# Kernel tuning notes

Hardware: AMD Instinct MI355X
Metric: run time of the kernel (lower is better)

## Reference

```python
import jax, jax.numpy as jnp
import numpy as np

N = 100000   # nodes
D = 128      # feature dim (in == hidden)
R = 3        # num edge types (relations)
E = 500000   # edges per relation
B = 2        # num bases


def setup_inputs() -> dict:
    key = jax.random.key(0)
    ks = jax.random.split(key, 12)
    s = 1.0 / np.sqrt(D)  # xavier-ish scale
    return {
        "x": jax.random.normal(ks[0], (N, D), jnp.float32),
        "edge_src": jax.random.randint(ks[1], (R, E), 0, N, dtype=jnp.int32),
        "edge_dst": jax.random.randint(ks[2], (R, E), 0, N, dtype=jnp.int32),
        "proj_w": jax.random.normal(ks[3], (D, D), jnp.float32) * s,
        "proj_b": jnp.zeros((D,), jnp.float32),
        "basis1": jax.random.normal(ks[4], (B, D, D), jnp.float32) * s,
        "coeff1": jax.random.normal(ks[5], (R, B), jnp.float32),
        "bias1": jnp.zeros((D,), jnp.float32),
        "loop1": jax.random.normal(ks[6], (D, D), jnp.float32) * s,
        "basis2": jax.random.normal(ks[7], (B, D, D), jnp.float32) * s,
        "coeff2": jax.random.normal(ks[8], (R, B), jnp.float32),
        "bias2": jnp.zeros((D,), jnp.float32),
        "loop2": jax.random.normal(ks[9], (D, D), jnp.float32) * s,
    }


def rel_graph_conv_layer(x, edge_src, edge_dst, basis, coeff, bias, loop_w):
    """RelGraphConvLayer: per-relation GraphConv(norm='right') + basis weights
    + self-loop + bias + relu. x: [N, D]."""
    # Offset dst ids per relation so one segment_sum covers all R relations.
    seg = (edge_dst + jnp.arange(R, dtype=edge_dst.dtype)[:, None] * N).reshape(-1)  # [R*E]
    gathered = x[edge_src.reshape(-1)]  # [R*E, D]
    agg = jax.ops.segment_sum(gathered, seg, num_segments=R * N).reshape(R, N, D)
    deg = jax.ops.segment_sum(jnp.ones((R * E,), x.dtype), seg, num_segments=R * N).reshape(R, N, 1)
    agg = agg / jnp.maximum(deg, 1.0)  # norm='right': 1/in_degree, clamped to >=1
    W = jnp.einsum('rb,bio->rio', coeff, basis)          # basis decomposition [R, D, D]
    h = jnp.einsum('rnd,rdo->no', agg, W)                # sum over relations (HeteroGraphConv 'sum')
    h = h + x @ loop_w + bias                            # self-loop + bias
    return jax.nn.relu(h)


def reference(x, edge_src, edge_dst, proj_w, proj_b,
              basis1, coeff1, bias1, loop1,
              basis2, coeff2, bias2, loop2):
    h = x @ proj_w + proj_b  # per-ntype projection layer
    h = rel_graph_conv_layer(h, edge_src, edge_dst, basis1, coeff1, bias1, loop1)
    h = rel_graph_conv_layer(h, edge_src, edge_dst, basis2, coeff2, bias2, loop2)
    return h
```

## Files before the change

### kernel.cpp

```cpp
#include <hip/hip_runtime.h>

typedef unsigned int uint;
typedef unsigned short ushort;
typedef __attribute__((ext_vector_type(8))) short bf16x8;
typedef __attribute__((ext_vector_type(4))) float f32x4;

namespace {
constexpr int kN = 100000;
constexpr int kD = 128;
constexpr int kR = 3;
constexpr int kE = 500000;
constexpr int kB = 2;
constexpr int kRN = kR * kN;
constexpr int kRE = kR * kE;
constexpr int kKS = kR * kD;
constexpr int kKC = kD + kKS;
constexpr int kNBK = (kN + 511) / 512;
constexpr int kNQ = kR * kNBK;
constexpr int kCB = (kRE + 2047) / 2048;
constexpr int kBCAP = 4096;
constexpr int kICAP = 5120;
}

__device__ __forceinline__ ushort f2bf(float f) {
    uint u = __builtin_bit_cast(uint, f);
    u += 0x7fff + ((u >> 16) & 1);
    return (ushort)(u >> 16);
}
__device__ __forceinline__ float bf2f(ushort h) {
    return __builtin_bit_cast(float, (uint)h << 16);
}
__device__ __forceinline__ int rel_of(int i) {
    return (i >= kE) + (i >= 2 * kE);
}

__device__ __forceinline__ void gload16(const void* g, void* l) {
    __builtin_amdgcn_global_load_lds(
        (__attribute__((address_space(1))) void*)(g),
        (__attribute__((address_space(3))) void*)(l),
        16, 0, 0);
}

__global__ __launch_bounds__(256)
void init_kernel(unsigned* __restrict__ bcur)
{
    const int q = blockIdx.x * 256 + threadIdx.x;
    if (q < kNQ) bcur[q] = (unsigned)q * kBCAP;
}

__global__ __launch_bounds__(256)
void f2bf_kernel(const float* __restrict__ in, ushort* __restrict__ out)
{
    const int i = blockIdx.x * 256 + threadIdx.x;
    const float4 v = ((const float4*)in)[i];
    ushort4 o;
    o.x = f2bf(v.x); o.y = f2bf(v.y); o.z = f2bf(v.z); o.w = f2bf(v.w);
    ((ushort4*)out)[i] = o;
}

__global__ __launch_bounds__(256)
void passB_kernel(const int* __restrict__ src, const int* __restrict__ dst,
                  unsigned* __restrict__ bcur, uint* __restrict__ colbkt)
{
    __shared__ unsigned bl[kNQ];
    __shared__ unsigned base_l[kNQ];
    const int tid = threadIdx.x;
    for (int q = tid; q < kNQ; q += 256) bl[q] = 0;
    __syncthreads();
    const int i0 = blockIdx.x * 2048 + tid * 8;
    int dd[8], qq[8];
    const bool full = (i0 + 8 <= kRE);
    if (full) {
        const int4 d0 = *(const int4*)(dst + i0);
        const int4 d1 = *(const int4*)(dst + i0 + 4);
        dd[0]=d0.x; dd[1]=d0.y; dd[2]=d0.z; dd[3]=d0.w;
        dd[4]=d1.x; dd[5]=d1.y; dd[6]=d1.z; dd[7]=d1.w;
        #pragma unroll
        for (int j = 0; j < 8; ++j) {
            qq[j] = rel_of(i0 + j) * kNBK + (dd[j] >> 9);
            atomicAdd(&bl[qq[j]], 1u);
        }
    } else {
        for (int j = 0; j < 8; ++j) {
            const int i = i0 + j;
            qq[j] = -1;
            if (i < kRE) {
                dd[j] = dst[i];
                qq[j] = rel_of(i) * kNBK + (dd[j] >> 9);
                atomicAdd(&bl[qq[j]], 1u);
            }
        }
    }
    __syncthreads();
    for (int q = tid; q < kNQ; q += 256) {
        const unsigned c = bl[q];
        base_l[q] = c ? atomicAdd(&bcur[q], c) : 0u;
        bl[q] = 0;
    }
    __syncthreads();
    if (full) {
        const int4 s0 = *(const int4*)(src + i0);
        const int4 s1 = *(const int4*)(src + i0 + 4);
        const int ss[8] = {s0.x, s0.y, s0.z, s0.w, s1.x, s1.y, s1.z, s1.w};
        #pragma unroll
        for (int j = 0; j < 8; ++j) {
            const unsigned pos = base_l[qq[j]] + atomicAdd(&bl[qq[j]], 1u);
            colbkt[pos] = ((uint)ss[j] << 9) | (uint)(dd[j] & 511);
        }
    } else {
        for (int j = 0; j < 8; ++j) {
            if (qq[j] >= 0) {
                const unsigned pos = base_l[qq[j]] + atomicAdd(&bl[qq[j]], 1u);
                colbkt[pos] = ((uint)src[i0 + j] << 9) | (uint)(dd[j] & 511);
            }
        }
    }
}

__global__ __launch_bounds__(256)
void passC_kernel(const uint* __restrict__ colbkt, const unsigned* __restrict__ bcur,
                  uint2* __restrict__ rowseg, float* __restrict__ invd,
                  int* __restrict__ colidx)
{
    __shared__ unsigned cnt[512];
    __shared__ unsigned pos[512];
    __shared__ unsigned psc[256];
    const int tid = threadIdx.x;
    const int q = blockIdx.x;
    const int r = q / kNBK;
    const int b = q - r * kNBK;
    const int n0 = b << 9;
    const int nn = min(512, kN - n0);
    cnt[tid] = 0; cnt[tid + 256] = 0;
    __syncthreads();
    const unsigned e0 = (unsigned)q * kBCAP;
    const unsigned e1 = bcur[q];
    for (unsigned j = e0 + tid; j < e1; j += 256)
        atomicAdd(&cnt[colbkt[j] & 511u], 1u);
    __syncthreads();
    const unsigned c0 = cnt[2 * tid], c1 = cnt[2 * tid + 1];
    const unsigned c0p = (c0 + 3u) & ~3u, c1p = (c1 + 3u) & ~3u;
    const unsigned psum = c0p + c1p;
    psc[tid] = psum;
    __syncthreads();
    #pragma unroll
    for (int off = 1; off < 256; off <<= 1) {
        unsigned t = (tid >= off) ? psc[tid - off] : 0u;
        __syncthreads();
        psc[tid] += t;
        __syncthreads();
    }
    const unsigned pex = psc[tid] - psum;
    const unsigned beg0 = (unsigned)q * kICAP + pex;
    const unsigned beg1 = beg0 + c0p;
    pos[2 * tid] = beg0;
    pos[2 * tid + 1] = beg1;
    const int g0 = 2 * tid, g1 = 2 * tid + 1;
    if (g0 < nn) {
        rowseg[(size_t)r * kN + n0 + g0] = make_uint2(beg0, beg0 + c0p);
        invd[(size_t)r * kN + n0 + g0] = 1.0f / (float)(c0 > 1u ? c0 : 1u);
        for (unsigned u = c0; u < c0p; ++u) colidx[beg0 + u] = kN;
    }
    if (g1 < nn) {
        rowseg[(size_t)r * kN + n0 + g1] = make_uint2(beg1, beg1 + c1p);
        invd[(size_t)r * kN + n0 + g1] = 1.0f / (float)(c1 > 1u ? c1 : 1u);
        for (unsigned u = c1; u < c1p; ++u) colidx[beg1 + u] = kN;
    }
    __syncthreads();
    for (unsigned j = e0 + tid; j < e1; j += 256) {
        const uint p = colbkt[j];
        const unsigned pp = atomicAdd(&pos[p & 511u], 1u);
        colidx[pp] = (int)(p >> 9);
    }
}

__device__ __forceinline__ void wcomb_one(int i, const float* loopW, const float* basis,
                                          const float* coeff, ushort* WTc)
{
    int out = i >> 9;
    int k = i & (kKC - 1);
    float v;
    if (k < kD) {
        v = loopW[(size_t)k * kD + out];
    } else {
        int j = k - kD;
        int r = j >> 7, d = j & 127;
        v = coeff[r * kB] * basis[(size_t)d * kD + out]
          + coeff[r * kB + 1] * basis[(size_t)kD * kD + d * kD + out];
    }
    WTc[i] = f2bf(v);
}

__global__ __launch_bounds__(256)
void prep_kernel(const float* __restrict__ proj_w,
                 const float* __restrict__ loop1, const float* __restrict__ basis1,
                 const float* __restrict__ coeff1,
                 const float* __restrict__ loop2, const float* __restrict__ basis2,
                 const float* __restrict__ coeff2,
                 ushort* __restrict__ WTp, ushort* __restrict__ WTc1,
                 ushort* __restrict__ WTc2,
                 ushort* __restrict__ hbZero, ushort* __restrict__ r1bZero)
{
    const int b = blockIdx.x;
    const int tid = threadIdx.x;
    if (b < 64) {
        const int i = b * 256 + tid;
        const int out = i >> 7, k = i & 127;
        WTp[i] = f2bf(proj_w[(size_t)k * kD + out]);
    } else if (b < 320) {
        wcomb_one((b - 64) * 256 + tid, loop1, basis1, coeff1, WTc1);
    } else if (b < 576) {
        wcomb_one((b - 320) * 256 + tid, loop2, basis2, coeff2, WTc2);
    } else if (b == 576) {
        if (tid < kD) hbZero[tid] = 0;
    } else {
        if (tid < kD) r1bZero[tid] = 0;
    }
}

__device__ __forceinline__ void acc8(float* s, uint4 v) {
    s[0] += bf2f((ushort)(v.x & 0xffffu)); s[1] += bf2f((ushort)(v.x >> 16));
    s[2] += bf2f((ushort)(v.y & 0xffffu)); s[3] += bf2f((ushort)(v.y >> 16));
    s[4] += bf2f((ushort)(v.z & 0xffffu)); s[5] += bf2f((ushort)(v.z >> 16));
    s[6] += bf2f((ushort)(v.w & 0xffffu)); s[7] += bf2f((ushort)(v.w >> 16));
}

__global__ __launch_bounds__(256)
void gather_kernel(const ushort* __restrict__ in, const uint2* __restrict__ rowseg,
                   const int* __restrict__ colidx, const float* __restrict__ invd,
                   ushort* __restrict__ a)
{
    const int tid = threadIdx.x;
    const int g   = tid >> 3;
    const int c   = tid & 7;
    const int seg = blockIdx.x * 32 + g;
    const int r = seg / kN;
    const int n = seg - r * kN;
    const uint2 be = rowseg[seg];

    float s[16];
    #pragma unroll
    for (int i = 0; i < 16; ++i) s[i] = 0.f;

    for (unsigned j = be.x; j < be.y; j += 4) {
        const int4 e = *(const int4*)(colidx + j);
        const ushort* p0 = in + (size_t)e.x * kD + c * 16;
        const ushort* p1 = in + (size_t)e.y * kD + c * 16;
        const ushort* p2 = in + (size_t)e.z * kD + c * 16;
        const ushort* p3 = in + (size_t)e.w * kD + c * 16;
        const uint4 v00 = *(const uint4*)p0;
        const uint4 v01 = *(const uint4*)(p0 + 8);
        const uint4 v10 = *(const uint4*)p1;
        const uint4 v11 = *(const uint4*)(p1 + 8);
        const uint4 v20 = *(const uint4*)p2;
        const uint4 v21 = *(const uint4*)(p2 + 8);
        const uint4 v30 = *(const uint4*)p3;
        const uint4 v31 = *(const uint4*)(p3 + 8);
        acc8(s, v00); acc8(s + 8, v01);
        acc8(s, v10); acc8(s + 8, v11);
        acc8(s, v20); acc8(s + 8, v21);
        acc8(s, v30); acc8(s + 8, v31);
    }

    const float w = invd[seg];
    uint4 o0, o1;
    o0.x = (uint)f2bf(s[0] * w)  | ((uint)f2bf(s[1] * w)  << 16);
    o0.y = (uint)f2bf(s[2] * w)  | ((uint)f2bf(s[3] * w)  << 16);
    o0.z = (uint)f2bf(s[4] * w)  | ((uint)f2bf(s[5] * w)  << 16);
    o0.w = (uint)f2bf(s[6] * w)  | ((uint)f2bf(s[7] * w)  << 16);
    o1.x = (uint)f2bf(s[8] * w)  | ((uint)f2bf(s[9] * w)  << 16);
    o1.y = (uint)f2bf(s[10] * w) | ((uint)f2bf(s[11] * w) << 16);
    o1.z = (uint)f2bf(s[12] * w) | ((uint)f2bf(s[13] * w) << 16);
    o1.w = (uint)f2bf(s[14] * w) | ((uint)f2bf(s[15] * w) << 16);
    ushort* ap = a + (size_t)n * kKS + r * kD + c * 16;
    *(uint4*)ap       = o0;
    *(uint4*)(ap + 8) = o1;
}

template<int NT0, int NT, bool RELUOUT, bool OUTBF16>
__global__ __launch_bounds__(256)
void mfma_gemm(const ushort* __restrict__ A0, const ushort* __restrict__ A1,
               const ushort* __restrict__ WT, const float* __restrict__ bias,
               void* __restrict__ Cout, int M)
{
    __shared__ ushort As[2][128 * 64];
    __shared__ ushort Bs[2][128 * 64];
    const int tid  = threadIdx.x;
    const int bm   = blockIdx.x * 128;
    const int lane = tid & 63;
    const int w    = tid >> 6;
    const int wbase = w << 6;
    const int wrow = (w >> 1) * 64;
    const int wcol = (w & 1) * 64;

    f32x4 acc[4][4];
    #pragma unroll
    for (int i = 0; i < 4; ++i)
        #pragma unroll
        for (int j = 0; j < 4; ++j)
            acc[i][j] = (f32x4){0.f, 0.f, 0.f, 0.f};

    auto stage = [&](int kt, int buf) {
        #pragma unroll
        for (int st = 0; st < 4; ++st) {
            const int m = st * 256 + tid;
            const int row = m >> 3;
            const int osrc = (m & 7) ^ (row & 7);
            int arow = bm + row; if (arow >= M) arow = M - 1;
            const ushort* ga = (kt < NT0)
                ? A0 + (size_t)arow * (NT0 * 64) + kt * 64 + osrc * 8
                : A1 + (size_t)arow * ((NT - NT0) * 64) + (kt - NT0) * 64 + osrc * 8;
            gload16(ga, &As[buf][(st * 256 + wbase) * 8]);
            const ushort* gb = WT + (size_t)row * (NT * 64) + kt * 64 + osrc * 8;
            gload16(gb, &Bs[buf][(st * 256 + wbase) * 8]);
        }
    };

    stage(0, 0);
    __syncthreads();
    #pragma unroll
    for (int kt = 0; kt < NT; ++kt) {
        const int buf = kt & 1;
        if (kt + 1 < NT) stage(kt + 1, buf ^ 1);

        #pragma unroll
        for (int ks = 0; ks < 2; ++ks) {
            const int oq = ks * 4 + (lane >> 4);
            bf16x8 af[4], bfr[4];
            #pragma unroll
            for (int am = 0; am < 4; ++am) {
                const int row = wrow + am * 16 + (lane & 15);
                const int oL = oq ^ (row & 7);
                af[am] = *(const bf16x8*)&As[buf][row * 64 + oL * 8];
            }
            #pragma unroll
            for (int bn = 0; bn < 4; ++bn) {
                const int row = wcol + bn * 16 + (lane & 15);
                const int oL = oq ^ (row & 7);
                bfr[bn] = *(const bf16x8*)&Bs[buf][row * 64 + oL * 8];
            }
            #pragma unroll
            for (int am = 0; am < 4; ++am)
                #pragma unroll
                for (int bn = 0; bn < 4; ++bn)
                    acc[am][bn] = __builtin_amdgcn_mfma_f32_16x16x32_bf16(
                        af[am], bfr[bn], acc[am][bn], 0, 0, 0);
        }
        __syncthreads();
    }

    const int ccol = wcol + (lane & 15);
    float bb[4];
    #pragma unroll
    for (int bn = 0; bn < 4; ++bn) bb[bn] = bias[ccol + bn * 16];

    const int crow0 = bm + wrow + 4 * (lane >> 4);
    #pragma unroll
    for (int am = 0; am < 4; ++am) {
        #pragma unroll
        for (int r = 0; r < 4; ++r) {
            const int row = crow0 + am * 16 + r;
            if (row < M) {
                #pragma unroll
                for (int bn = 0; bn < 4; ++bn) {
                    float v = acc[am][bn][r] + bb[bn];
                    if (RELUOUT) v = fmaxf(v, 0.f);
                    if (OUTBF16)
                        ((ushort*)Cout)[(size_t)row * kD + ccol + bn * 16] = f2bf(v);
                    else
                        ((float*)Cout)[(size_t)row * kD + ccol + bn * 16] = v;
                }
            }
        }
    }
}

extern "C" void kernel_launch(void* const* d_in, const int* in_sizes, int n_in,
                              void* d_out, int out_size, void* d_ws, size_t ws_size,
                              hipStream_t stream)
{
    const float* x      = (const float*)d_in[0];
    const int*   esrc   = (const int*)d_in[1];
    const int*   edst   = (const int*)d_in[2];
    const float* proj_w = (const float*)d_in[3];
    const float* proj_b = (const float*)d_in[4];
    const float* basis1 = (const float*)d_in[5];
    const float* coeff1 = (const float*)d_in[6];
    const float* bias1  = (const float*)d_in[7];
    const float* loop1  = (const float*)d_in[8];
    const float* basis2 = (const float*)d_in[9];
    const float* coeff2 = (const float*)d_in[10];
    const float* bias2  = (const float*)d_in[11];
    const float* loop2  = (const float*)d_in[12];

    char* p = (char*)d_ws;
    ushort* xb    = (ushort*)p;  p += (size_t)kN * kD * 2;
    ushort* hb    = (ushort*)p;  p += (size_t)(kN + 1) * kD * 2;
    ushort* r1b   = (ushort*)p;  p += (size_t)(kN + 1) * kD * 2;
    ushort* ab    = (ushort*)p;  p += (size_t)kN * kKS * 2;
    ushort* WTp   = (ushort*)p;  p += (size_t)kD * kD * 2;
    ushort* WTc1  = (ushort*)p;  p += (size_t)kD * kKC * 2;
    ushort* WTc2  = (ushort*)p;  p += (size_t)kD * kKC * 2;
    float* invd   = (float*)p;   p += (size_t)kRN * 4;
    uint2* rowseg = (uint2*)p;   p += (size_t)kRN * 8;
    unsigned* bcur = (unsigned*)p;  p += (size_t)kNQ * 4;
    uint* colbkt   = (uint*)p;      p += (size_t)kNQ * kBCAP * 4;
    int* colidx    = (int*)p;       p += (size_t)kNQ * kICAP * 4;

    init_kernel<<<(kNQ + 255) / 256, 256, 0, stream>>>(bcur);
    passB_kernel<<<kCB, 256, 0, stream>>>(esrc, edst, bcur, colbkt);
    passC_kernel<<<kNQ, 256, 0, stream>>>(colbkt, bcur, rowseg, invd, colidx);

    prep_kernel<<<578, 256, 0, stream>>>(proj_w, loop1, basis1, coeff1,
                                         loop2, basis2, coeff2, WTp, WTc1, WTc2,
                                         hb + (size_t)kN * kD, r1b + (size_t)kN * kD);
    f2bf_kernel<<<(kN * kD / 4) / 256, 256, 0, stream>>>(x, xb);

    const int gblocks = (kN + 127) / 128;
    const int gatherblocks = kRN / 32;

    mfma_gemm<2, 2, false, true><<<gblocks, 256, 0, stream>>>(
        xb, nullptr, WTp, proj_b, hb, kN);

    gather_kernel<<<gatherblocks, 256, 0, stream>>>(hb, rowseg, colidx, invd, ab);
    mfma_gemm<2, 8, true, true><<<gblocks, 256, 0, stream>>>(
        hb, ab, WTc1, bias1, r1b, kN);

    gather_kernel<<<gatherblocks, 256, 0, stream>>>(r1b, rowseg, colidx, invd, ab);
    mfma_gemm<2, 8, true, false><<<gblocks, 256, 0, stream>>>(
        r1b, ab, WTc2, bias2, d_out, kN);
}
```

Measured before the change: 357.0 us.

## Restructure GEMM to stage full-K A tile in LDS and read weights from global

The MFMA GEMM now works on 64-row tiles. It loads the entire K extent of the A tile into shared memory once, replacing the double-buffered K-tile loop. Weight fragments are read straight from global memory (cached in L2) rather than staged through LDS, and each wave now covers a 64x32 output slice. This drops the per-K-step syncthreads and the LDS traffic for B, and doubles the block count. In exchange, LDS use is up to 64 KB per block, which can cut occupancy, there is no overlap between loads and compute, and B reads become uncoalesced global loads.

```diff
diff --git a/kernel.cpp b/kernel.cpp
--- a/kernel.cpp
+++ b/kernel.cpp
@@ -277,84 +277,85 @@
     *(uint4*)(ap + 8) = o1;
 }
 
-template<int NT0, int NT, bool RELUOUT, bool OUTBF16>
+template<int K0, int K1, bool RELUOUT, bool OUTBF16>
 __global__ __launch_bounds__(256)
 void mfma_gemm(const ushort* __restrict__ A0, const ushort* __restrict__ A1,
                const ushort* __restrict__ WT, const float* __restrict__ bias,
                void* __restrict__ Cout, int M)
 {
-    __shared__ ushort As[2][128 * 64];
-    __shared__ ushort Bs[2][128 * 64];
-    const int tid  = threadIdx.x;
-    const int bm   = blockIdx.x * 128;
-    const int lane = tid & 63;
-    const int w    = tid >> 6;
+    constexpr int KTOT = K0 + K1;
+    constexpr int CPR  = KTOT / 8;
+    constexpr int NST  = 64 * CPR / 256;
+    __shared__ ushort As[64 * KTOT];
+
+    const int tid   = threadIdx.x;
+    const int bm    = blockIdx.x * 64;
+    const int lane  = tid & 63;
+    const int w     = tid >> 6;
     const int wbase = w << 6;
-    const int wrow = (w >> 1) * 64;
-    const int wcol = (w & 1) * 64;
-
-    f32x4 acc[4][4];
+    const int wcol  = w * 32;
+
+    #pragma unroll
+    for (int st = 0; st < NST; ++st) {
+        const int m    = st * 256 + tid;
+        const int row  = m / CPR;
+        const int cir  = m & (CPR - 1);
+        const int gg   = cir >> 3;
+        const int oL   = cir & 7;
+        const int osrc = oL ^ (row & 7);
+        const int kcol = gg * 64 + osrc * 8;
+        int arow = bm + row; if (arow >= M) arow = M - 1;
+        const ushort* ga = (K1 == 0 || kcol < K0)
+            ? A0 + (size_t)arow * K0 + kcol
+            : A1 + (size_t)arow * K1 + (kcol - K0);
+        gload16(ga, &As[(st * 256 + wbase) * 8]);
+    }
+    __syncthreads();
+
+    f32x4 acc[4][2];
     #pragma unroll
     for (int i = 0; i < 4; ++i)
         #pragma unroll
-        for (int j = 0; j < 4; ++j)
+        for (int j = 0; j < 2; ++j)
             acc[i][j] = (f32x4){0.f, 0.f, 0.f, 0.f};
 
-    auto stage = [&](int kt, int buf) {
-        #pragma unroll
-        for (int st = 0; st < 4; ++st) {
-            const int m = st * 256 + tid;
-            const int row = m >> 3;
-            const int osrc = (m & 7) ^ (row & 7);
-            int arow = bm + row; if (arow >= M) arow = M - 1;
-            const ushort* ga = (kt < NT0)
-                ? A0 + (size_t)arow * (NT0 * 64) + kt * 64 + osrc * 8
-                : A1 + (size_t)arow * ((NT - NT0) * 64) + (kt - NT0) * 64 + osrc * 8;
-            gload16(ga, &As[buf][(st * 256 + wbase) * 8]);
-            const ushort* gb = WT + (size_t)row * (NT * 64) + kt * 64 + osrc * 8;
-            gload16(gb, &Bs[buf][(st * 256 + wbase) * 8]);
-        }
-    };
-
-    stage(0, 0);
-    __syncthreads();
-    #pragma unroll
-    for (int kt = 0; kt < NT; ++kt) {
-        const int buf = kt & 1;
-        if (kt + 1 < NT) stage(kt + 1, buf ^ 1);
-
+    #pragma unroll
+    for (int g = 0; g < KTOT / 64; ++g) {
+        bf16x8 bfr[2][2];
         #pragma unroll
         for (int ks = 0; ks < 2; ++ks) {
             const int oq = ks * 4 + (lane >> 4);
-            bf16x8 af[4], bfr[4];
+            #pragma unroll
+            for (int bn = 0; bn < 2; ++bn) {
+                const int brow = wcol + bn * 16 + (lane & 15);
+                bfr[ks][bn] = *(const bf16x8*)(WT + (size_t)brow * KTOT + g * 64 + oq * 8);
+            }
+        }
+        #pragma unroll
+        for (int ks = 0; ks < 2; ++ks) {
+            const int oq = ks * 4 + (lane >> 4);
+            bf16x8 af[4];
             #pragma unroll
             for (int am = 0; am < 4; ++am) {
-                const int row = wrow + am * 16 + (lane & 15);
+                const int row = am * 16 + (lane & 15);
                 const int oL = oq ^ (row & 7);
-                af[am] = *(const bf16x8*)&As[buf][row * 64 + oL * 8];
-            }
-            #pragma unroll
-            for (int bn = 0; bn < 4; ++bn) {
-                const int row = wcol + bn * 16 + (lane & 15);
-                const int oL = oq ^ (row & 7);
-                bfr[bn] = *(const bf16x8*)&Bs[buf][row * 64 + oL * 8];
+                af[am] = *(const bf16x8*)&As[row * KTOT + (g * 8 + oL) * 8];
             }
             #pragma unroll
             for (int am = 0; am < 4; ++am)
                 #pragma unroll
-                for (int bn = 0; bn < 4; ++bn)
+                for (int bn = 0; bn < 2; ++bn)
                     acc[am][bn] = __builtin_amdgcn_mfma_f32_16x16x32_bf16(
-                        af[am], bfr[bn], acc[am][bn], 0, 0, 0);
-        }
-        __syncthreads();
+                        af[am], bfr[ks][bn], acc[am][bn], 0, 0, 0);
+        }
     }
 
     const int ccol = wcol + (lane & 15);
-    float bb[4];
-    #pragma unroll
-    for (int bn = 0; bn < 4; ++bn) bb[bn] = bias[ccol + bn * 16];
-
-    const int crow0 = bm + wrow + 4 * (lane >> 4);
+    float bb[2];
+    #pragma unroll
+    for (int bn = 0; bn < 2; ++bn) bb[bn] = bias[ccol + bn * 16];
+
+    const int crow0 = bm + 4 * (lane >> 4);
     #pragma unroll
     for (int am = 0; am < 4; ++am) {
         #pragma unroll
@@ -362,7 +363,7 @@
             const int row = crow0 + am * 16 + r;
             if (row < M) {
                 #pragma unroll
-                for (int bn = 0; bn < 4; ++bn) {
+                for (int bn = 0; bn < 2; ++bn) {
                     float v = acc[am][bn][r] + bb[bn];
                     if (RELUOUT) v = fmaxf(v, 0.f);
                     if (OUTBF16)
@@ -416,17 +417,17 @@
                                          hb + (size_t)kN * kD, r1b + (size_t)kN * kD);
     f2bf_kernel<<<(kN * kD / 4) / 256, 256, 0, stream>>>(x, xb);
 
-    const int gblocks = (kN + 127) / 128;
+    const int gblocks = (kN + 63) / 64;
     const int gatherblocks = kRN / 32;
 
-    mfma_gemm<2, 2, false, true><<<gblocks, 256, 0, stream>>>(
+    mfma_gemm<128, 0, false, true><<<gblocks, 256, 0, stream>>>(
         xb, nullptr, WTp, proj_b, hb, kN);
 
     gather_kernel<<<gatherblocks, 256, 0, stream>>>(hb, rowseg, colidx, invd, ab);
-    mfma_gemm<2, 8, true, true><<<gblocks, 256, 0, stream>>>(
+    mfma_gemm<128, 384, true, true><<<gblocks, 256, 0, stream>>>(
         hb, ab, WTc1, bias1, r1b, kN);
 
     gather_kernel<<<gatherblocks, 256, 0, stream>>>(r1b, rowseg, colidx, invd, ab);
-    mfma_gemm<2, 8, true, false><<<gblocks, 256, 0, stream>>>(
+    mfma_gemm<128, 384, true, false><<<gblocks, 256, 0, stream>>>(
         r1b, ab, WTc2, bias2, d_out, kN);
 }
```

Result: slower. 412.0 us (+15.4%).
